# Kernel optimization log

Hardware: AMD Instinct MI355X
Metric: run time of the kernel (lower is better)

## Reference

```python
import jax, jax.numpy as jnp
import numpy as np

D = 256          # d_model
NH = 8           # n_heads
HD = D // NH
LEV = 3          # n_levels
NP = 4           # n_points
DFF = 1024       # d_ffn
B = 8            # batch
LQ = 3600        # 60*60 queries (hardcoded in get_reference_points)
SHAPES = np.array([[60, 60], [30, 30], [15, 15]], dtype=np.int64)
LIN = int((SHAPES[:, 0] * SHAPES[:, 1]).sum())  # 4725
START = np.concatenate([[0], np.cumsum(SHAPES[:, 0] * SHAPES[:, 1])[:-1]]).astype(np.int64)


def setup_inputs() -> dict:
    key = jax.random.key(0)
    ks = iter(jax.random.split(key, 32))
    def lin(k, o, i):
        return jax.random.normal(k, (o, i), jnp.float32) * 0.02
    return {
        "tgt": jax.random.normal(next(ks), (LQ, B, D), jnp.float32),
        "query_pos": jax.random.normal(next(ks), (1, 1, D), jnp.float32),
        "src": jax.random.normal(next(ks), (B, LIN, D), jnp.float32),
        "src_spatial_shapes": jnp.asarray(SHAPES),
        "level_start_index": jnp.asarray(START),
        "in_proj_w": lin(next(ks), 3 * D, D),
        "in_proj_b": jnp.zeros((3 * D,), jnp.float32),
        "out_proj_w": lin(next(ks), D, D),
        "out_proj_b": jnp.zeros((D,), jnp.float32),
        "samp_off_w": lin(next(ks), NH * LEV * NP * 2, D),
        "samp_off_b": jax.random.normal(next(ks), (NH * LEV * NP * 2,), jnp.float32) * 0.5,
        "attn_w_w": lin(next(ks), NH * LEV * NP, D),
        "attn_w_b": jnp.zeros((NH * LEV * NP,), jnp.float32),
        "value_proj_w": lin(next(ks), D, D),
        "value_proj_b": jnp.zeros((D,), jnp.float32),
        "cross_out_w": lin(next(ks), D, D),
        "cross_out_b": jnp.zeros((D,), jnp.float32),
        "ln1_g": jnp.ones((D,), jnp.float32), "ln1_b": jnp.zeros((D,), jnp.float32),
        "ln2_g": jnp.ones((D,), jnp.float32), "ln2_b": jnp.zeros((D,), jnp.float32),
        "ln3_g": jnp.ones((D,), jnp.float32), "ln3_b": jnp.zeros((D,), jnp.float32),
        "ffn_w1": lin(next(ks), DFF, D), "ffn_b1": jnp.zeros((DFF,), jnp.float32),
        "ffn_w2": lin(next(ks), D, DFF), "ffn_b2": jnp.zeros((D,), jnp.float32),
    }


def _ln(x, g, b, eps=1e-5):
    m = x.mean(-1, keepdims=True)
    v = ((x - m) ** 2).mean(-1, keepdims=True)
    return (x - m) * jax.lax.rsqrt(v + eps) * g + b


def _self_attn(q_in, k_in, v_in, wqkv, bqkv, wo, bo):
    # torch nn.MultiheadAttention semantics, inputs laid out (seq, batch, embed)
    S, N, _ = q_in.shape
    q = (q_in @ wqkv[:D].T + bqkv[:D]).reshape(S, N, NH, HD)
    k = (k_in @ wqkv[D:2 * D].T + bqkv[D:2 * D]).reshape(S, N, NH, HD)
    v = (v_in @ wqkv[2 * D:].T + bqkv[2 * D:]).reshape(S, N, NH, HD)
    logits = jnp.einsum('snhd,tnhd->nhst', q, k) / np.sqrt(HD).astype(np.float32)
    a = jax.nn.softmax(logits, -1)
    ctx = jnp.einsum('nhst,tnhd->snhd', a, v).reshape(S, N, D)
    return ctx @ wo.T + bo


def _bilinear(v_l, loc, Hl, Wl):
    # v_l: [B, NH, Hl*Wl, HD]; loc: [B, NH, LQ, NP, 2] normalized in [0,1]
    # grid_sample(align_corners=False, padding=zeros): pixel = loc*size - 0.5
    x = loc[..., 0] * Wl - 0.5
    y = loc[..., 1] * Hl - 0.5
    x0 = jnp.floor(x); y0 = jnp.floor(y)
    fx = x - x0; fy = y - y0
    x0 = x0.astype(jnp.int32); y0 = y0.astype(jnp.int32)
    def corner(yi, xi, w):
        valid = ((xi >= 0) & (xi < Wl) & (yi >= 0) & (yi < Hl)).astype(v_l.dtype)
        idx = jnp.clip(yi, 0, Hl - 1) * Wl + jnp.clip(xi, 0, Wl - 1)
        b, h, lq, p = idx.shape
        g = jnp.take_along_axis(v_l, idx.reshape(b, h, lq * p)[..., None], axis=2)
        return g.reshape(b, h, lq, p, HD) * (w * valid)[..., None]
    return (corner(y0, x0, (1 - fx) * (1 - fy))
            + corner(y0, x0 + 1, fx * (1 - fy))
            + corner(y0 + 1, x0, (1 - fx) * fy)
            + corner(y0 + 1, x0 + 1, fx * fy))


def _msdeform(query, ref, src, wso, bso, waw, baw, wv, bv, wo, bo):
    Bq, Lq, _ = query.shape
    value = (src @ wv.T + bv).reshape(Bq, LIN, NH, HD).transpose(0, 2, 1, 3)  # [B,NH,LIN,HD]
    off = (query @ wso.T + bso).reshape(Bq, Lq, NH, LEV, NP, 2)
    aw = (query @ waw.T + baw).reshape(Bq, Lq, NH, LEV * NP)
    aw = jax.nn.softmax(aw, -1).reshape(Bq, Lq, NH, LEV, NP)
    normalizer = jnp.asarray(SHAPES[:, ::-1].copy(), jnp.float32)  # (W, H) per level
    loc = ref[:, :, None, :, None, :] + off / normalizer[None, None, None, :, None, :]
    out = jnp.zeros((Bq, NH, Lq, HD), query.dtype)
    for l in range(LEV):
        Hl, Wl = int(SHAPES[l, 0]), int(SHAPES[l, 1])
        s = int(START[l])
        v_l = value[:, :, s:s + Hl * Wl]
        loc_l = loc[:, :, :, l].transpose(0, 2, 1, 3, 4)      # [B,NH,LQ,NP,2]
        sampled = _bilinear(v_l, loc_l, Hl, Wl)               # [B,NH,LQ,NP,HD]
        out = out + (sampled * aw[:, :, :, l].transpose(0, 2, 1, 3)[..., None]).sum(3)
    out = out.transpose(0, 2, 1, 3).reshape(Bq, Lq, D)
    return out @ wo.T + bo


def _reference_points():
    Hh = Ww = 60
    ys = (jnp.arange(Hh, dtype=jnp.float32) + 0.5) / Hh
    xs = (jnp.arange(Ww, dtype=jnp.float32) + 0.5) / Ww
    yy, xx = jnp.meshgrid(ys, xs, indexing='ij')
    ref = jnp.stack([xx.reshape(-1), yy.reshape(-1)], -1)[None]  # [1, 3600, 2]
    return jnp.broadcast_to(ref[:, :, None, :], (1, Hh * Ww, LEV, 2))


def reference(tgt, query_pos, src, src_spatial_shapes, level_start_index,
              in_proj_w, in_proj_b, out_proj_w, out_proj_b,
              samp_off_w, samp_off_b, attn_w_w, attn_w_b,
              value_proj_w, value_proj_b, cross_out_w, cross_out_b,
              ln1_g, ln1_b, ln2_g, ln2_b, ln3_g, ln3_b,
              ffn_w1, ffn_b1, ffn_w2, ffn_b2):
    # dropout layers are identity (eval mode). spatial shapes are static metadata
    # (SHAPES/START) since slicing sizes must be static under jit.
    q = (tgt + query_pos).transpose(1, 0, 2)
    tgt2 = _self_attn(q, q, tgt.transpose(1, 0, 2), in_proj_w, in_proj_b, out_proj_w, out_proj_b)
    t = _ln(tgt + tgt2.transpose(1, 0, 2), ln2_g, ln2_b)
    ref = _reference_points()
    tq = t.transpose(1, 0, 2)  # permute(1,0,2) -> [B, LQ, D]
    tgt2 = _msdeform(tq + query_pos, ref, src, samp_off_w, samp_off_b,
                     attn_w_w, attn_w_b, value_proj_w, value_proj_b,
                     cross_out_w, cross_out_b)
    tq = _ln(tq + tgt2, ln1_g, ln1_b)
    ff = jax.nn.relu(tq @ ffn_w1.T + ffn_b1) @ ffn_w2.T + ffn_b2
    tq = _ln(tq + ff, ln3_g, ln3_b)
    return tq.transpose(1, 0, 2)  # [LQ, B, D]
```

## Files before the change

### kernel.cpp

```cpp
#include <hip/hip_runtime.h>
#include <hip/hip_bf16.h>
#include <cstddef>
#include <cstdint>

#define D_MODEL 256
#define NHEAD   8
#define HDIM    32
#define NLEV    3
#define NPNT    4
#define DFF     1024
#define BATCH   8
#define LQ      3600
#define LIN     4725
#define MROWS   (BATCH*LQ)

typedef short bf16x8 __attribute__((ext_vector_type(8)));
typedef float f32x4  __attribute__((ext_vector_type(4)));

__device__ __forceinline__ unsigned short f2b(float x) {
    unsigned int u = __float_as_uint(x);
    unsigned int r = (u + 0x7fffu + ((u >> 16) & 1u)) >> 16;
    return (unsigned short)r;
}
__device__ __forceinline__ float b2f(unsigned short s) {
    return __uint_as_float(((unsigned int)s) << 16);
}

#define GLDS16(g, l) __builtin_amdgcn_global_load_lds( \
    (const __attribute__((address_space(1))) void*)(g), \
    (__attribute__((address_space(3))) void*)(l), 16, 0, 0)

#define WAIT_VM0()  asm volatile("s_waitcnt vmcnt(0)" ::: "memory")
#define WAIT_LGKM0() asm volatile("s_waitcnt lgkmcnt(0)" ::: "memory")

#define WTOT 991232
__global__ __launch_bounds__(256) void prep_kernel(
    const float* __restrict__ tgt, unsigned short* __restrict__ tgtb,
    const float* __restrict__ srcf, unsigned short* __restrict__ srcb,
    const float* __restrict__ w_in, const float* __restrict__ w_out,
    const float* __restrict__ w_val, const float* __restrict__ w_cross,
    const float* __restrict__ w_so, const float* __restrict__ w_aw,
    const float* __restrict__ w_f1, const float* __restrict__ w_f2,
    unsigned short* __restrict__ wdst,
    const float* __restrict__ qp, const float* __restrict__ so_b,
    const float* __restrict__ aw_b, float* __restrict__ qpv)
{
    const int bid = blockIdx.x;
    const int tid = threadIdx.x;
    if (bid < 7200) {
        int i = bid * 256 + tid;
        float4 v = ((const float4*)tgt)[i];
        ushort4 o; o.x = f2b(v.x); o.y = f2b(v.y); o.z = f2b(v.z); o.w = f2b(v.w);
        ((ushort4*)tgtb)[i] = o;
    } else if (bid < 16650) {
        int i = (bid - 7200) * 256 + tid;
        float4 v = ((const float4*)srcf)[i];
        ushort4 o; o.x = f2b(v.x); o.y = f2b(v.y); o.z = f2b(v.z); o.w = f2b(v.w);
        ((ushort4*)srcb)[i] = o;
    } else if (bid < 17618) {
        int idx = ((bid - 16650) * 256 + tid) * 4;
        if (idx >= WTOT) return;
        const float* src; int off;
        if      (idx < 196608) { src = w_in;    off = idx; }
        else if (idx < 262144) { src = w_out;   off = idx - 196608; }
        else if (idx < 327680) { src = w_val;   off = idx - 262144; }
        else if (idx < 393216) { src = w_cross; off = idx - 327680; }
        else if (idx < 442368) { src = w_so;    off = idx - 393216; }
        else if (idx < 466944) { src = w_aw;    off = idx - 442368; }
        else if (idx < 729088) { src = w_f1;    off = idx - 466944; }
        else                   { src = w_f2;    off = idx - 729088; }
        float4 v = *(const float4*)(src + off);
        ushort4 o; o.x = f2b(v.x); o.y = f2b(v.y); o.z = f2b(v.z); o.w = f2b(v.w);
        *(ushort4*)(wdst + idx) = o;
    } else {
        int o = (bid - 17618) * 256 + tid;
        if (o >= 768 + 192 + 96) return;
        const float* wrow;
        if (o < 768)       wrow = w_in + (size_t)o * D_MODEL;
        else if (o < 960)  wrow = w_so + (size_t)(o - 768) * D_MODEL;
        else               wrow = w_aw + (size_t)(o - 960) * D_MODEL;
        float acc = 0.f;
        for (int d = 0; d < D_MODEL; ++d) acc += qp[d] * wrow[d];
        qpv[o] = acc;
        if (o >= 768) {
            float bias = (o < 960) ? so_b[o - 768] : aw_b[o - 960];
            qpv[1056 + (o - 768)] = acc + bias;
        }
    }
}

__global__ __launch_bounds__(256) void gemm_bf16(
    const unsigned short* __restrict__ A,
    const unsigned short* __restrict__ W,
    const float* __restrict__ bias,
    const float* __restrict__ bias2, int b2lim,
    float* __restrict__ Cf, unsigned short* __restrict__ Cb,
    int M, int N, int K, int relu)
{
    __shared__ __align__(16) unsigned short As[2 * 128 * 32];
    __shared__ __align__(16) unsigned short Bs[2 * 128 * 32];
    const int tid  = threadIdx.x;
    const int wave = tid >> 6;
    const int lane = tid & 63;
    const int m0 = blockIdx.x * 128;
    const int n0 = blockIdx.y * 128;

    const int lr  = lane >> 2;
    const int lc8 = (lane & 3) * 8;
    int ar0 = m0 + wave * 32 + lr;      if (ar0 > M - 1) ar0 = M - 1;
    int ar1 = m0 + wave * 32 + 16 + lr; if (ar1 > M - 1) ar1 = M - 1;
    int br0 = n0 + wave * 32 + lr;      if (br0 > N - 1) br0 = N - 1;
    int br1 = n0 + wave * 32 + 16 + lr; if (br1 > N - 1) br1 = N - 1;
    const unsigned short* pa0 = A + (size_t)ar0 * K + lc8;
    const unsigned short* pa1 = A + (size_t)ar1 * K + lc8;
    const unsigned short* pb0 = W + (size_t)br0 * K + lc8;
    const unsigned short* pb1 = W + (size_t)br1 * K + lc8;
    unsigned short* la0 = As + wave * 1024;
    unsigned short* la1 = As + wave * 1024 + 512;
    unsigned short* lb0 = Bs + wave * 1024;
    unsigned short* lb1 = Bs + wave * 1024 + 512;

    const int wm = (wave >> 1) * 64;
    const int wn = (wave & 1) * 64;
    const int fr = lane & 15;
    const int fk = (lane >> 4) * 8;

    f32x4 acc[4][4] = {};

    for (int k0 = 0; k0 < K; k0 += 64) {
        GLDS16(pa0, la0); GLDS16(pa0 + 32, la0 + 4096);
        GLDS16(pa1, la1); GLDS16(pa1 + 32, la1 + 4096);
        GLDS16(pb0, lb0); GLDS16(pb0 + 32, lb0 + 4096);
        GLDS16(pb1, lb1); GLDS16(pb1 + 32, lb1 + 4096);
        pa0 += 64; pa1 += 64; pb0 += 64; pb1 += 64;
        __syncthreads();
#pragma unroll
        for (int p = 0; p < 2; ++p) {
            bf16x8 af[4], bfv[4];
#pragma unroll
            for (int i = 0; i < 4; ++i)
                af[i] = *(const bf16x8*)&As[p * 4096 + (wm + i * 16 + fr) * 32 + fk];
#pragma unroll
            for (int j = 0; j < 4; ++j)
                bfv[j] = *(const bf16x8*)&Bs[p * 4096 + (wn + j * 16 + fr) * 32 + fk];
#pragma unroll
            for (int i = 0; i < 4; ++i)
#pragma unroll
                for (int j = 0; j < 4; ++j)
                    acc[i][j] = __builtin_amdgcn_mfma_f32_16x16x32_bf16(
                        af[i], bfv[j], acc[i][j], 0, 0, 0);
        }
        __syncthreads();
    }

    const int quad = lane >> 4;
#pragma unroll
    for (int j = 0; j < 4; ++j) {
        const int col = n0 + wn + j * 16 + fr;
        if (col >= N) continue;
        float bv = 0.f;
        if (bias) bv += bias[col];
        if (bias2 && col < b2lim) bv += bias2[col];
#pragma unroll
        for (int i = 0; i < 4; ++i) {
#pragma unroll
            for (int r = 0; r < 4; ++r) {
                const int row = m0 + wm + i * 16 + quad * 4 + r;
                if (row >= M) continue;
                float v = acc[i][j][r] + bv;
                if (relu) v = fmaxf(v, 0.f);
                if (Cf) Cf[(size_t)row * N + col] = v;
                if (Cb) Cb[(size_t)row * N + col] = f2b(v);
            }
        }
    }
}

__global__ __launch_bounds__(256) void ln2_offs_kernel(
    const unsigned short* __restrict__ A,
    const unsigned short* __restrict__ Wo,
    const float* __restrict__ bo,
    const float* __restrict__ resid,
    const float* __restrict__ g2, const float* __restrict__ b2g,
    float* __restrict__ tout,
    const unsigned short* __restrict__ Wso,
    const float* __restrict__ cbias,
    float* __restrict__ comb)
{
    __shared__ __align__(16) unsigned short Wc[16384];
    __shared__ float2 red[128];
    const int tid  = threadIdx.x;
    const int wave = tid >> 6;
    const int lane = tid & 63;
    const int m0 = blockIdx.x * 32;
    const int fr   = lane & 15;
    const int quad = lane >> 4;
    const int xm   = fr & 7;

#pragma unroll
    for (int j = 0; j < 4; ++j) {
        const int c  = wave * 4 + j;
        const int rA = c * 2 + (lane >> 5);
        const int k8 = (lane & 31) ^ (rA & 7);
        GLDS16(A + (size_t)(m0 + rA) * 256 + k8 * 8, Wc + c * 512);
    }
    int w1off[8], w4off[8];
#pragma unroll
    for (int j = 0; j < 8; ++j) {
        const int c  = wave * 8 + j;
        const int n1 = c * 2 + (lane >> 5);
        const int k1 = (lane & 31) ^ (n1 & 7);
        w1off[j] = n1 * 256 + k1 * 8;
        const int n4 = (n1 < 32) ? n1 : 31;
        const int k4 = (lane & 31) ^ (n4 & 7);
        w4off[j] = n4 * 256 + k4 * 8;
    }
    __syncthreads();
    bf16x8 af[2][8];
#pragma unroll
    for (int i = 0; i < 2; ++i)
#pragma unroll
        for (int s = 0; s < 8; ++s)
            af[i][s] = *(const bf16x8*)&Wc[((i * 16 + fr) * 32 + ((s * 4 + quad) ^ xm)) * 8];
    WAIT_LGKM0();
    __syncthreads();

#pragma unroll
    for (int j = 0; j < 8; ++j)
        GLDS16(Wo + w1off[j], Wc + (wave * 8 + j) * 512);
    f32x4 accc[4][2] = {};
    for (int c = 0; c < 4; ++c) {
        WAIT_VM0();
        bf16x8 bv[8];
#pragma unroll
        for (int s = 0; s < 8; ++s)
            bv[s] = *(const bf16x8*)&Wc[((wave * 16 + fr) * 32 + ((s * 4 + quad) ^ xm)) * 8];
        WAIT_LGKM0();
        if (c < 3) {
#pragma unroll
            for (int j = 0; j < 8; ++j)
                GLDS16(Wo + (size_t)(c + 1) * 16384 + w1off[j], Wc + (wave * 8 + j) * 512);
        }
#pragma unroll
        for (int s = 0; s < 8; ++s) {
            accc[c][0] = __builtin_amdgcn_mfma_f32_16x16x32_bf16(af[0][s], bv[s], accc[c][0], 0, 0, 0);
            accc[c][1] = __builtin_amdgcn_mfma_f32_16x16x32_bf16(af[1][s], bv[s], accc[c][1], 0, 0, 0);
        }
    }

    float rs[2][4], rq[2][4];
#pragma unroll
    for (int x = 0; x < 2; ++x) {
#pragma unroll
        for (int r = 0; r < 4; ++r) {
            const int row = m0 + x * 16 + quad * 4 + r;
            float s = 0.f, q = 0.f;
#pragma unroll
            for (int c = 0; c < 4; ++c) {
                const int col = c * 64 + wave * 16 + fr;
                float v = accc[c][x][r] + bo[col] + resid[(size_t)row * 256 + col];
                accc[c][x][r] = v;
                s += v; q += v * v;
            }
            rs[x][r] = s; rq[x][r] = q;
        }
    }
#pragma unroll
    for (int off = 1; off < 16; off <<= 1) {
#pragma unroll
        for (int x = 0; x < 2; ++x)
#pragma unroll
            for (int r = 0; r < 4; ++r) {
                rs[x][r] += __shfl_xor(rs[x][r], off);
                rq[x][r] += __shfl_xor(rq[x][r], off);
            }
    }
    if ((lane & 15) == 0) {
#pragma unroll
        for (int x = 0; x < 2; ++x)
#pragma unroll
            for (int r = 0; r < 4; ++r)
                red[wave * 32 + x * 16 + quad * 4 + r] = make_float2(rs[x][r], rq[x][r]);
    }
    __syncthreads();
#pragma unroll
    for (int x = 0; x < 2; ++x) {
#pragma unroll
        for (int r = 0; r < 4; ++r) {
            const int rl = x * 16 + quad * 4 + r;
            const float2 t0 = red[rl], t1 = red[32 + rl], t2r = red[64 + rl], t3 = red[96 + rl];
            const float sum = t0.x + t1.x + t2r.x + t3.x;
            const float sq  = t0.y + t1.y + t2r.y + t3.y;
            const float mean = sum * (1.f / 256.f);
            const float var  = sq * (1.f / 256.f) - mean * mean;
            const float inv  = rsqrtf(var + 1e-5f);
            const int row = m0 + rl;
#pragma unroll
            for (int c = 0; c < 4; ++c) {
                const int col = c * 64 + wave * 16 + fr;
                const float val = (accc[c][x][r] - mean) * inv * g2[col] + b2g[col];
                tout[(size_t)row * 256 + col] = val;
                const int g8 = col >> 3;
                Wc[rl * 256 + ((g8 ^ (rl & 7)) << 3) + (col & 7)] = f2b(val);
            }
        }
    }
    __syncthreads();
#pragma unroll
    for (int i = 0; i < 2; ++i)
#pragma unroll
        for (int s = 0; s < 8; ++s)
            af[i][s] = *(const bf16x8*)&Wc[((i * 16 + fr) * 32 + ((s * 4 + quad) ^ xm)) * 8];
    WAIT_LGKM0();
    __syncthreads();

#pragma unroll
    for (int j = 0; j < 8; ++j)
        GLDS16(Wso + w1off[j], Wc + (wave * 8 + j) * 512);
    f32x4 accP[5][2] = {};
    for (int c = 0; c < 5; ++c) {
        WAIT_VM0();
        bf16x8 bv[8];
#pragma unroll
        for (int s = 0; s < 8; ++s)
            bv[s] = *(const bf16x8*)&Wc[((wave * 16 + fr) * 32 + ((s * 4 + quad) ^ xm)) * 8];
        WAIT_LGKM0();
        if (c < 4) {
            if (c < 3) {
#pragma unroll
                for (int j = 0; j < 8; ++j)
                    GLDS16(Wso + (size_t)(c + 1) * 16384 + w1off[j], Wc + (wave * 8 + j) * 512);
            } else {
#pragma unroll
                for (int j = 0; j < 8; ++j)
                    GLDS16(Wso + (size_t)4 * 16384 + w4off[j], Wc + (wave * 8 + j) * 512);
            }
        }
#pragma unroll
        for (int s = 0; s < 8; ++s) {
            accP[c][0] = __builtin_amdgcn_mfma_f32_16x16x32_bf16(af[0][s], bv[s], accP[c][0], 0, 0, 0);
            accP[c][1] = __builtin_amdgcn_mfma_f32_16x16x32_bf16(af[1][s], bv[s], accP[c][1], 0, 0, 0);
        }
    }

#pragma unroll
    for (int c = 0; c < 5; ++c) {
        const int col = c * 64 + wave * 16 + fr;
        if (col >= 288) continue;
        const float cb = cbias[col];
#pragma unroll
        for (int x = 0; x < 2; ++x)
#pragma unroll
            for (int r = 0; r < 4; ++r) {
                const int row = m0 + x * 16 + quad * 4 + r;
                comb[(size_t)row * 288 + col] = accP[c][x][r] + cb;
            }
    }
}

__global__ __launch_bounds__(256) void cross_ffn_kernel(
    const unsigned short* __restrict__ A,
    const unsigned short* __restrict__ Wcr,
    const float* __restrict__ bcr,
    const float* __restrict__ resid1,
    const float* __restrict__ g1, const float* __restrict__ b1g,
    float* __restrict__ t2,
    const unsigned short* __restrict__ W1,
    const float* __restrict__ b1,
    const unsigned short* __restrict__ W2,
    const float* __restrict__ b2,
    const float* __restrict__ g3, const float* __restrict__ b3g,
    float* __restrict__ outf)
{
    __shared__ __align__(16) unsigned short Wc[16384];
    __shared__ __align__(16) unsigned short hid[2304];
    const int tid  = threadIdx.x;
    const int wave = tid >> 6;
    const int lane = tid & 63;
    const int m0 = blockIdx.x * 32;
    const int fr   = lane & 15;
    const int quad = lane >> 4;
    const int xm   = fr & 7;
    float2* red = (float2*)hid;

#pragma unroll
    for (int j = 0; j < 4; ++j) {
        const int c  = wave * 4 + j;
        const int rA = c * 2 + (lane >> 5);
        const int k8 = (lane & 31) ^ (rA & 7);
        GLDS16(A + (size_t)(m0 + rA) * 256 + k8 * 8, Wc + c * 512);
    }
    int w1off[8], w2off[8];
#pragma unroll
    for (int j = 0; j < 8; ++j) {
        const int c  = wave * 8 + j;
        const int n1 = c * 2 + (lane >> 5);
        const int k1 = (lane & 31) ^ (n1 & 7);
        w1off[j] = n1 * 256 + k1 * 8;
        const int n2 = c * 8 + (lane >> 3);
        const int k2 = (lane & 7) ^ (n2 & 7);
        w2off[j] = n2 * 1024 + k2 * 8;
    }
    __syncthreads();
    bf16x8 af[2][8];
#pragma unroll
    for (int i = 0; i < 2; ++i)
#pragma unroll
        for (int s = 0; s < 8; ++s)
            af[i][s] = *(const bf16x8*)&Wc[((i * 16 + fr) * 32 + ((s * 4 + quad) ^ xm)) * 8];
    WAIT_LGKM0();
    __syncthreads();

#pragma unroll
    for (int j = 0; j < 8; ++j)
        GLDS16(Wcr + w1off[j], Wc + (wave * 8 + j) * 512);
    f32x4 accc[4][2] = {};
    for (int c = 0; c < 4; ++c) {
        WAIT_VM0();
        bf16x8 bv[8];
#pragma unroll
        for (int s = 0; s < 8; ++s)
            bv[s] = *(const bf16x8*)&Wc[((wave * 16 + fr) * 32 + ((s * 4 + quad) ^ xm)) * 8];
        WAIT_LGKM0();
        if (c < 3) {
#pragma unroll
            for (int j = 0; j < 8; ++j)
                GLDS16(Wcr + (size_t)(c + 1) * 16384 + w1off[j], Wc + (wave * 8 + j) * 512);
        }
#pragma unroll
        for (int s = 0; s < 8; ++s) {
            accc[c][0] = __builtin_amdgcn_mfma_f32_16x16x32_bf16(af[0][s], bv[s], accc[c][0], 0, 0, 0);
            accc[c][1] = __builtin_amdgcn_mfma_f32_16x16x32_bf16(af[1][s], bv[s], accc[c][1], 0, 0, 0);
        }
    }

    float rs[2][4], rq[2][4];
#pragma unroll
    for (int x = 0; x < 2; ++x) {
#pragma unroll
        for (int r = 0; r < 4; ++r) {
            const int row = m0 + x * 16 + quad * 4 + r;
            float s = 0.f, q = 0.f;
#pragma unroll
            for (int c = 0; c < 4; ++c) {
                const int col = c * 64 + wave * 16 + fr;
                float v = accc[c][x][r] + bcr[col] + resid1[(size_t)row * 256 + col];
                accc[c][x][r] = v;
                s += v; q += v * v;
            }
            rs[x][r] = s; rq[x][r] = q;
        }
    }
#pragma unroll
    for (int off = 1; off < 16; off <<= 1) {
#pragma unroll
        for (int x = 0; x < 2; ++x)
#pragma unroll
            for (int r = 0; r < 4; ++r) {
                rs[x][r] += __shfl_xor(rs[x][r], off);
                rq[x][r] += __shfl_xor(rq[x][r], off);
            }
    }
    if ((lane & 15) == 0) {
#pragma unroll
        for (int x = 0; x < 2; ++x)
#pragma unroll
            for (int r = 0; r < 4; ++r)
                red[wave * 32 + x * 16 + quad * 4 + r] = make_float2(rs[x][r], rq[x][r]);
    }
    __syncthreads();
#pragma unroll
    for (int x = 0; x < 2; ++x) {
#pragma unroll
        for (int r = 0; r < 4; ++r) {
            const int rl = x * 16 + quad * 4 + r;
            const float2 t0 = red[rl], t1 = red[32 + rl], t2r = red[64 + rl], t3 = red[96 + rl];
            const float sum = t0.x + t1.x + t2r.x + t3.x;
            const float sq  = t0.y + t1.y + t2r.y + t3.y;
            const float mean = sum * (1.f / 256.f);
            const float var  = sq * (1.f / 256.f) - mean * mean;
            const float inv  = rsqrtf(var + 1e-5f);
            const int row = m0 + rl;
#pragma unroll
            for (int c = 0; c < 4; ++c) {
                const int col = c * 64 + wave * 16 + fr;
                const float val = (accc[c][x][r] - mean) * inv * g1[col] + b1g[col];
                t2[(size_t)row * 256 + col] = val;
                const int g8 = col >> 3;
                Wc[rl * 256 + ((g8 ^ (rl & 7)) << 3) + (col & 7)] = f2b(val);
            }
        }
    }
    __syncthreads();
#pragma unroll
    for (int i = 0; i < 2; ++i)
#pragma unroll
        for (int s = 0; s < 8; ++s)
            af[i][s] = *(const bf16x8*)&Wc[((i * 16 + fr) * 32 + ((s * 4 + quad) ^ xm)) * 8];
    WAIT_LGKM0();
    __syncthreads();

#pragma unroll
    for (int j = 0; j < 8; ++j)
        GLDS16(W1 + w1off[j], Wc + (wave * 8 + j) * 512);
    WAIT_VM0();

    f32x4 acc2[2][4] = {};

    for (int h = 0; h < 16; ++h) {
        bf16x8 bv[8];
#pragma unroll
        for (int s = 0; s < 8; ++s)
            bv[s] = *(const bf16x8*)&Wc[((wave * 16 + fr) * 32 + ((s * 4 + quad) ^ xm)) * 8];
        WAIT_LGKM0();
#pragma unroll
        for (int j = 0; j < 8; ++j)
            GLDS16(W2 + (size_t)h * 64 + w2off[j], Wc + (wave * 8 + j) * 512);
        f32x4 acc1[2] = {};
#pragma unroll
        for (int s = 0; s < 8; ++s) {
            acc1[0] = __builtin_amdgcn_mfma_f32_16x16x32_bf16(af[0][s], bv[s], acc1[0], 0, 0, 0);
            acc1[1] = __builtin_amdgcn_mfma_f32_16x16x32_bf16(af[1][s], bv[s], acc1[1], 0, 0, 0);
        }
        const float bias1 = b1[h * 64 + wave * 16 + fr];
#pragma unroll
        for (int i = 0; i < 2; ++i)
#pragma unroll
            for (int r = 0; r < 4; ++r) {
                float v = fmaxf(acc1[i][r] + bias1, 0.f);
                hid[(i * 16 + quad * 4 + r) * 72 + wave * 16 + fr] = f2b(v);
            }
        __syncthreads();
#pragma unroll
        for (int s = 0; s < 2; ++s) {
            bf16x8 a2[2], b2v[4];
#pragma unroll
            for (int j2 = 0; j2 < 4; ++j2) {
                const int nb = wave * 64 + j2 * 16 + fr;
                b2v[j2] = *(const bf16x8*)&Wc[(nb * 8 + ((s * 4 + quad) ^ xm)) * 8];
            }
#pragma unroll
            for (int i = 0; i < 2; ++i)
                a2[i] = *(const bf16x8*)&hid[(i * 16 + fr) * 72 + s * 32 + quad * 8];
            if (s == 1) {
                WAIT_LGKM0();
                if (h < 15) {
#pragma unroll
                    for (int j = 0; j < 8; ++j)
                        GLDS16(W1 + (size_t)(h + 1) * 16384 + w1off[j], Wc + (wave * 8 + j) * 512);
                }
            }
#pragma unroll
            for (int i = 0; i < 2; ++i)
#pragma unroll
                for (int j2 = 0; j2 < 4; ++j2)
                    acc2[i][j2] = __builtin_amdgcn_mfma_f32_16x16x32_bf16(
                        a2[i], b2v[j2], acc2[i][j2], 0, 0, 0);
        }
        __syncthreads();
    }

    const int colbase = wave * 64;
#pragma unroll
    for (int x = 0; x < 2; ++x) {
#pragma unroll
        for (int r = 0; r < 4; ++r) {
            const int row = m0 + x * 16 + quad * 4 + r;
            float s = 0.f, q = 0.f;
#pragma unroll
            for (int y = 0; y < 4; ++y) {
                const int col = colbase + y * 16 + fr;
                float v = acc2[x][y][r] + b2[col] + t2[(size_t)row * 256 + col];
                acc2[x][y][r] = v;
                s += v; q += v * v;
            }
            rs[x][r] = s; rq[x][r] = q;
        }
    }
#pragma unroll
    for (int off = 1; off < 16; off <<= 1) {
#pragma unroll
        for (int x = 0; x < 2; ++x)
#pragma unroll
            for (int r = 0; r < 4; ++r) {
                rs[x][r] += __shfl_xor(rs[x][r], off);
                rq[x][r] += __shfl_xor(rq[x][r], off);
            }
    }
    if ((lane & 15) == 0) {
#pragma unroll
        for (int x = 0; x < 2; ++x)
#pragma unroll
            for (int r = 0; r < 4; ++r)
                red[wave * 32 + x * 16 + quad * 4 + r] = make_float2(rs[x][r], rq[x][r]);
    }
    __syncthreads();
#pragma unroll
    for (int x = 0; x < 2; ++x) {
#pragma unroll
        for (int r = 0; r < 4; ++r) {
            const int rl = x * 16 + quad * 4 + r;
            const float2 t0 = red[rl], t1 = red[32 + rl], t2r = red[64 + rl], t3 = red[96 + rl];
            const float sum = t0.x + t1.x + t2r.x + t3.x;
            const float sq  = t0.y + t1.y + t2r.y + t3.y;
            const float mean = sum * (1.f / 256.f);
            const float var  = sq * (1.f / 256.f) - mean * mean;
            const float inv  = rsqrtf(var + 1e-5f);
            const int row = m0 + rl;
#pragma unroll
            for (int y = 0; y < 4; ++y) {
                const int col = colbase + y * 16 + fr;
                outf[(size_t)row * 256 + col] = (acc2[x][y][r] - mean) * inv * g3[col] + b3g[col];
            }
        }
    }
}

__global__ __launch_bounds__(256) void self_attn_kernel(
    const unsigned short* __restrict__ qkv, unsigned short* __restrict__ ctx)
{
    __shared__ float sh[8][768];
    __shared__ float ls[8][8][8];
    __shared__ __align__(16) unsigned short ob[2048];
    const int n = blockIdx.x;
    const int t = threadIdx.x;

    const unsigned short* base = qkv + (size_t)n * 8 * 768;
#pragma unroll
    for (int i = 0; i < 3; ++i) {
        const int idx = (i * 256 + t) * 8;
        bf16x8 v = *(const bf16x8*)&base[idx];
        const int s = idx / 768;
        const int c = idx - s * 768;
#pragma unroll
        for (int j = 0; j < 8; ++j)
            sh[s][c + j] = b2f((unsigned short)v[j]);
    }
    __syncthreads();
    const int h = t >> 5, j = t & 31;
#pragma unroll
    for (int pair = j; pair < 64; pair += 32) {
        const int s = pair >> 3, tt = pair & 7;
        float acc = 0.f;
#pragma unroll
        for (int d = 0; d < 32; ++d)
            acc += sh[s][h * 32 + d] * sh[tt][256 + h * 32 + d];
        ls[h][s][tt] = acc * 0.17677669529663687f;
    }
    __syncthreads();
    if (t < 64) {
        const int hh = t >> 3, s = t & 7;
        float mx = -1e30f;
        for (int tt = 0; tt < 8; ++tt) mx = fmaxf(mx, ls[hh][s][tt]);
        float sum = 0.f;
        for (int tt = 0; tt < 8; ++tt) { float e = expf(ls[hh][s][tt] - mx); ls[hh][s][tt] = e; sum += e; }
        const float inv = 1.f / sum;
        for (int tt = 0; tt < 8; ++tt) ls[hh][s][tt] *= inv;
    }
    __syncthreads();
#pragma unroll
    for (int s = 0; s < 8; ++s) {
        float acc = 0.f;
#pragma unroll
        for (int tt = 0; tt < 8; ++tt)
            acc += ls[h][s][tt] * sh[tt][512 + h * 32 + j];
        ob[s * 256 + t] = f2b(acc);
    }
    __syncthreads();
    ((bf16x8*)ctx)[(size_t)n * 256 + t] = ((const bf16x8*)ob)[t];
}

__global__ __launch_bounds__(256) void msdeform_kernel(
    const unsigned short* __restrict__ value,
    const float* __restrict__ comb,
    unsigned short* __restrict__ out)
{
    const int bid = blockIdx.x;
    const int b   = bid & 7;
    const int lq0 = (bid >> 3) * 4;
    const int r    = threadIdx.x >> 6;
    const int lane = threadIdx.x & 63;
    const int h = lane >> 3;
    const int l = lane & 7;
    const int lq = lq0 + r;
    const int m = lq * 8 + b;

    const float* offp = comb + (size_t)m * 288 + h * 24;
    const float* awp  = comb + (size_t)m * 288 + 192 + h * 12;
    float off[24], aw[12];
#pragma unroll
    for (int i = 0; i < 6; ++i) *(float4*)&off[i * 4] = ((const float4*)offp)[i];
#pragma unroll
    for (int i = 0; i < 3; ++i) *(float4*)&aw[i * 4] = ((const float4*)awp)[i];

    float mx = aw[0];
#pragma unroll
    for (int i = 1; i < 12; ++i) mx = fmaxf(mx, aw[i]);
    float se = 0.f;
#pragma unroll
    for (int i = 0; i < 12; ++i) { aw[i] = __expf(aw[i] - mx); se += aw[i]; }
    const float inv = 1.f / se;

    const float refx = ((lq % 60) + 0.5f) * (1.f / 60.f);
    const float refy = ((lq / 60) + 0.5f) * (1.f / 60.f);
    const int HW[3] = {60, 30, 15};
    const int ST[3] = {0, 3600, 4500};

    const unsigned short* vbase = value + (size_t)b * LIN * 256 + h * 32 + l * 4;

    float a0 = 0.f, a1 = 0.f, a2 = 0.f, a3 = 0.f;
#pragma unroll
    for (int lev = 0; lev < NLEV; ++lev) {
        const int Wl = HW[lev], s0 = ST[lev];
        const float fWl = (float)Wl;
#pragma unroll
        for (int p = 0; p < NPNT; ++p) {
            const int pt = lev * 4 + p;
            const float ox = off[lev * 8 + p * 2];
            const float oy = off[lev * 8 + p * 2 + 1];
            const float px = refx * fWl + ox - 0.5f;
            const float py = refy * fWl + oy - 0.5f;
            const float x0f = floorf(px), y0f = floorf(py);
            const float fx = px - x0f, fy = py - y0f;
            const int x0 = (int)x0f, y0 = (int)y0f;
            const float aww = aw[pt] * inv;
            const float vx0 = (x0 >= 0 && x0 < Wl) ? 1.f : 0.f;
            const float vx1 = (x0 >= -1 && x0 < Wl - 1) ? 1.f : 0.f;
            const float vy0 = (y0 >= 0 && y0 < Wl) ? 1.f : 0.f;
            const float vy1 = (y0 >= -1 && y0 < Wl - 1) ? 1.f : 0.f;
            const int xc0 = min(max(x0, 0), Wl - 1);
            const int xc1 = min(max(x0 + 1, 0), Wl - 1);
            const int yc0 = min(max(y0, 0), Wl - 1);
            const int yc1 = min(max(y0 + 1, 0), Wl - 1);
            const int sx  = xc1 - xc0;
            const int syW = (yc1 - yc0) * Wl;
            const int i00 = s0 + yc0 * Wl + xc0;
            const float w00 = (1.f - fx) * (1.f - fy) * aww * vx0 * vy0;
            const float w01 = fx * (1.f - fy) * aww * vx1 * vy0;
            const float w10 = (1.f - fx) * fy * aww * vx0 * vy1;
            const float w11 = fx * fy * aww * vx1 * vy1;
            const int i01 = i00 + sx;
            const int i10 = i00 + syW;
            const int i11 = i10 + sx;
            const ushort4 g00 = *(const ushort4*)(vbase + (size_t)i00 * 256);
            const ushort4 g01 = *(const ushort4*)(vbase + (size_t)i01 * 256);
            const ushort4 g10 = *(const ushort4*)(vbase + (size_t)i10 * 256);
            const ushort4 g11 = *(const ushort4*)(vbase + (size_t)i11 * 256);
            a0 += b2f(g00.x) * w00 + b2f(g01.x) * w01 + b2f(g10.x) * w10 + b2f(g11.x) * w11;
            a1 += b2f(g00.y) * w00 + b2f(g01.y) * w01 + b2f(g10.y) * w10 + b2f(g11.y) * w11;
            a2 += b2f(g00.z) * w00 + b2f(g01.z) * w01 + b2f(g10.z) * w10 + b2f(g11.z) * w11;
            a3 += b2f(g00.w) * w00 + b2f(g01.w) * w01 + b2f(g10.w) * w10 + b2f(g11.w) * w11;
        }
    }
    ushort4 o;
    o.x = f2b(a0); o.y = f2b(a1); o.z = f2b(a2); o.w = f2b(a3);
    *(ushort4*)(out + (size_t)m * 256 + h * 32 + l * 4) = o;
}

extern "C" void kernel_launch(void* const* d_in, const int* in_sizes, int n_in,
                              void* d_out, int out_size, void* d_ws, size_t ws_size,
                              hipStream_t stream)
{
    (void)in_sizes; (void)n_in; (void)out_size; (void)ws_size;
    const float* tgt          = (const float*)d_in[0];
    const float* qp           = (const float*)d_in[1];
    const float* src          = (const float*)d_in[2];
    const float* in_proj_w    = (const float*)d_in[5];
    const float* in_proj_b    = (const float*)d_in[6];
    const float* out_proj_w   = (const float*)d_in[7];
    const float* out_proj_b   = (const float*)d_in[8];
    const float* samp_off_w   = (const float*)d_in[9];
    const float* samp_off_b   = (const float*)d_in[10];
    const float* attn_w_w     = (const float*)d_in[11];
    const float* attn_w_b     = (const float*)d_in[12];
    const float* value_proj_w = (const float*)d_in[13];
    const float* value_proj_b = (const float*)d_in[14];
    const float* cross_out_w  = (const float*)d_in[15];
    const float* cross_out_b  = (const float*)d_in[16];
    const float* ln1_g = (const float*)d_in[17];
    const float* ln1_b = (const float*)d_in[18];
    const float* ln2_g = (const float*)d_in[19];
    const float* ln2_b = (const float*)d_in[20];
    const float* ln3_g = (const float*)d_in[21];
    const float* ln3_b = (const float*)d_in[22];
    const float* ffn_w1 = (const float*)d_in[23];
    const float* ffn_b1 = (const float*)d_in[24];
    const float* ffn_w2 = (const float*)d_in[25];
    const float* ffn_b2 = (const float*)d_in[26];
    float* out = (float*)d_out;

    float* ws    = (float*)d_ws;
    float* t     = ws;
    float* t2    = ws + 7372800;
    float* comb  = ws + 14745600;
    float* qpv   = ws + 23040000;
    float* cbias = qpv + 1056;

    unsigned short* bws    = (unsigned short*)((char*)d_ws + 92165376);
    unsigned short* s1     = bws;
    unsigned short* tgtb   = s1;
    unsigned short* ctxb   = s1;
    unsigned short* s2     = bws + 7372800;
    unsigned short* qkvb   = s2;
    unsigned short* valueb = s2;
    unsigned short* msoutb = s2 + 9676800;
    unsigned short* srcb   = bws + 36864000;
    unsigned short* wtsb   = bws + 46540800;

    prep_kernel<<<17623, 256, 0, stream>>>(tgt, tgtb, src, srcb,
                                           in_proj_w, out_proj_w, value_proj_w,
                                           cross_out_w, samp_off_w, attn_w_w,
                                           ffn_w1, ffn_w2, wtsb,
                                           qp, samp_off_b, attn_w_b, qpv);
    gemm_bf16<<<dim3(225, 6), 256, 0, stream>>>(tgtb, wtsb + 0, in_proj_b, qpv, 512,
                                                nullptr, qkvb, MROWS, 768, 256, 0);
    self_attn_kernel<<<3600, 256, 0, stream>>>(qkvb, ctxb);
    ln2_offs_kernel<<<900, 256, 0, stream>>>(ctxb, wtsb + 196608, out_proj_b,
                                             tgt, ln2_g, ln2_b, t,
                                             wtsb + 393216, cbias, comb);
    gemm_bf16<<<dim3(296, 2), 256, 0, stream>>>(srcb, wtsb + 262144, value_proj_b, nullptr, 0,
                                                nullptr, valueb, BATCH * LIN, 256, 256, 0);
    msdeform_kernel<<<7200, 256, 0, stream>>>(valueb, comb, msoutb);
    cross_ffn_kernel<<<900, 256, 0, stream>>>(msoutb, wtsb + 327680, cross_out_b,
                                              t, ln1_g, ln1_b, t2,
                                              wtsb + 466944, ffn_b1,
                                              wtsb + 729088, ffn_b2,
                                              ln3_g, ln3_b, out);
}
```

Measured before the change: 444.5 us.

## Fuse QKV projection and self-attention into the out-proj/LN2/offsets kernel

Moves the QKV GEMM and the 8-token per-query self-attention into the existing out-projection/LayerNorm/sampling-offset kernel, so each 32-row tile computes Q, K, V into shared memory and writes the attention context straight into the A-operand buffer. This drops two kernel launches and the global round trips for the QKV and context tensors. In exchange the fused kernel uses more shared memory (two extra 32x264 bf16 tiles), which may lower occupancy, and it runs the serial QKV chunks inside the block.

```diff
diff --git a/kernel.cpp b/kernel.cpp
--- a/kernel.cpp
+++ b/kernel.cpp
@@ -176,8 +176,11 @@
     }
 }
 
-__global__ __launch_bounds__(256) void ln2_offs_kernel(
+__global__ __launch_bounds__(256) void qkv_attn_ln2_offs_kernel(
     const unsigned short* __restrict__ A,
+    const unsigned short* __restrict__ Win,
+    const float* __restrict__ bin,
+    const float* __restrict__ qpv,
     const unsigned short* __restrict__ Wo,
     const float* __restrict__ bo,
     const float* __restrict__ resid,
@@ -188,6 +191,8 @@
     float* __restrict__ comb)
 {
     __shared__ __align__(16) unsigned short Wc[16384];
+    __shared__ __align__(16) unsigned short qt[32 * 264];
+    __shared__ __align__(16) unsigned short kvt[32 * 264];
     __shared__ float2 red[128];
     const int tid  = threadIdx.x;
     const int wave = tid >> 6;
@@ -227,6 +232,118 @@
 
 #pragma unroll
     for (int j = 0; j < 8; ++j)
+        GLDS16(Win + w1off[j], Wc + (wave * 8 + j) * 512);
+
+#define QCHUNK(CG, PF) {                                                     \
+        WAIT_VM0();                                                          \
+        bf16x8 bv[8];                                                        \
+        _Pragma("unroll")                                                    \
+        for (int s = 0; s < 8; ++s)                                          \
+            bv[s] = *(const bf16x8*)&Wc[((wave * 16 + fr) * 32 + ((s * 4 + quad) ^ xm)) * 8]; \
+        WAIT_LGKM0();                                                        \
+        if (PF) {                                                            \
+            _Pragma("unroll")                                                \
+            for (int j = 0; j < 8; ++j)                                      \
+                GLDS16(Win + (size_t)((CG) + 1) * 16384 + w1off[j], Wc + (wave * 8 + j) * 512); \
+        }                                                                    \
+        _Pragma("unroll")                                                    \
+        for (int s = 0; s < 8; ++s) {                                        \
+            acc[(CG) & 3][0] = __builtin_amdgcn_mfma_f32_16x16x32_bf16(af[0][s], bv[s], acc[(CG) & 3][0], 0, 0, 0); \
+            acc[(CG) & 3][1] = __builtin_amdgcn_mfma_f32_16x16x32_bf16(af[1][s], bv[s], acc[(CG) & 3][1], 0, 0, 0); \
+        }                                                                    \
+    }
+
+#define QKV_EPI(P, TILE) {                                                   \
+        _Pragma("unroll")                                                    \
+        for (int x = 0; x < 2; ++x)                                          \
+        _Pragma("unroll")                                                    \
+        for (int r = 0; r < 4; ++r) {                                        \
+            const int rl = x * 16 + quad * 4 + r;                            \
+            _Pragma("unroll")                                                \
+            for (int c = 0; c < 4; ++c) {                                    \
+                const int col  = c * 64 + wave * 16 + fr;                    \
+                const int gcol = (P) * 256 + col;                            \
+                float v = acc[c][x][r] + bin[gcol];                          \
+                if ((P) < 2) v += qpv[gcol];                                 \
+                (TILE)[rl * 264 + col] = f2b(v);                             \
+            }                                                                \
+        }                                                                    \
+    }
+
+    {
+        f32x4 acc[4][2] = {};
+#pragma unroll
+        for (int c = 0; c < 4; ++c) QCHUNK(c, 1)
+        QKV_EPI(0, qt)
+    }
+    {
+        f32x4 acc[4][2] = {};
+#pragma unroll
+        for (int c = 4; c < 8; ++c) QCHUNK(c, 1)
+        QKV_EPI(1, kvt)
+    }
+    __syncthreads();
+
+    const int g  = wave;
+    const int ah = lane >> 3;
+    const int si = lane & 7;
+    float p[8];
+    {
+        float qreg[32];
+#pragma unroll
+        for (int d = 0; d < 32; ++d)
+            qreg[d] = b2f(qt[(g * 8 + si) * 264 + ah * 32 + d]);
+        float mx = -1e30f;
+#pragma unroll
+        for (int ti = 0; ti < 8; ++ti) {
+            float a = 0.f;
+#pragma unroll
+            for (int d = 0; d < 32; ++d)
+                a += qreg[d] * b2f(kvt[(g * 8 + ti) * 264 + ah * 32 + d]);
+            a *= 0.17677669529663687f;
+            p[ti] = a;
+            mx = fmaxf(mx, a);
+        }
+        float sum = 0.f;
+#pragma unroll
+        for (int ti = 0; ti < 8; ++ti) { p[ti] = expf(p[ti] - mx); sum += p[ti]; }
+        const float inv = 1.f / sum;
+#pragma unroll
+        for (int ti = 0; ti < 8; ++ti) p[ti] *= inv;
+    }
+    __syncthreads();
+
+    {
+        f32x4 acc[4][2] = {};
+#pragma unroll
+        for (int c = 8; c < 12; ++c) QCHUNK(c, (c < 11))
+        QKV_EPI(2, kvt)
+    }
+    __syncthreads();
+
+    {
+        const int rl = g * 8 + si;
+#pragma unroll
+        for (int d = 0; d < 32; ++d) {
+            float a = 0.f;
+#pragma unroll
+            for (int ti = 0; ti < 8; ++ti)
+                a += p[ti] * b2f(kvt[(g * 8 + ti) * 264 + ah * 32 + d]);
+            const int col = ah * 32 + d;
+            Wc[rl * 256 + (((col >> 3) ^ (rl & 7)) << 3) + (col & 7)] = f2b(a);
+        }
+    }
+    __syncthreads();
+#pragma unroll
+    for (int i = 0; i < 2; ++i)
+#pragma unroll
+        for (int s = 0; s < 8; ++s)
+            af[i][s] = *(const bf16x8*)&Wc[((i * 16 + fr) * 32 + ((s * 4 + quad) ^ xm)) * 8];
+    WAIT_LGKM0();
+    __syncthreads();
+
+#pragma unroll
+    for (int j = 0; j < 8; ++j)
         GLDS16(Wo + w1off[j], Wc + (wave * 8 + j) * 512);
     f32x4 accc[4][2] = {};
     for (int c = 0; c < 4; ++c) {
@@ -247,7 +364,6 @@
             accc[c][1] = __builtin_amdgcn_mfma_f32_16x16x32_bf16(af[1][s], bv[s], accc[c][1], 0, 0, 0);
         }
     }
-
     float rs[2][4], rq[2][4];
 #pragma unroll
     for (int x = 0; x < 2; ++x) {
@@ -342,7 +458,6 @@
             accP[c][1] = __builtin_amdgcn_mfma_f32_16x16x32_bf16(af[1][s], bv[s], accP[c][1], 0, 0, 0);
         }
     }
-
 #pragma unroll
     for (int c = 0; c < 5; ++c) {
         const int col = c * 64 + wave * 16 + fr;
@@ -356,6 +471,8 @@
                 comb[(size_t)row * 288 + col] = accP[c][x][r] + cb;
             }
     }
+#undef QCHUNK
+#undef QKV_EPI
 }
 
 __global__ __launch_bounds__(256) void cross_ffn_kernel(
@@ -614,60 +731,6 @@
             }
         }
     }
-}
-
-__global__ __launch_bounds__(256) void self_attn_kernel(
-    const unsigned short* __restrict__ qkv, unsigned short* __restrict__ ctx)
-{
-    __shared__ float sh[8][768];
-    __shared__ float ls[8][8][8];
-    __shared__ __align__(16) unsigned short ob[2048];
-    const int n = blockIdx.x;
-    const int t = threadIdx.x;
-
-    const unsigned short* base = qkv + (size_t)n * 8 * 768;
-#pragma unroll
-    for (int i = 0; i < 3; ++i) {
-        const int idx = (i * 256 + t) * 8;
-        bf16x8 v = *(const bf16x8*)&base[idx];
-        const int s = idx / 768;
-        const int c = idx - s * 768;
-#pragma unroll
-        for (int j = 0; j < 8; ++j)
-            sh[s][c + j] = b2f((unsigned short)v[j]);
-    }
-    __syncthreads();
-    const int h = t >> 5, j = t & 31;
-#pragma unroll
-    for (int pair = j; pair < 64; pair += 32) {
-        const int s = pair >> 3, tt = pair & 7;
-        float acc = 0.f;
-#pragma unroll
-        for (int d = 0; d < 32; ++d)
-            acc += sh[s][h * 32 + d] * sh[tt][256 + h * 32 + d];
-        ls[h][s][tt] = acc * 0.17677669529663687f;
-    }
-    __syncthreads();
-    if (t < 64) {
-        const int hh = t >> 3, s = t & 7;
-        float mx = -1e30f;
-        for (int tt = 0; tt < 8; ++tt) mx = fmaxf(mx, ls[hh][s][tt]);
-        float sum = 0.f;
-        for (int tt = 0; tt < 8; ++tt) { float e = expf(ls[hh][s][tt] - mx); ls[hh][s][tt] = e; sum += e; }
-        const float inv = 1.f / sum;
-        for (int tt = 0; tt < 8; ++tt) ls[hh][s][tt] *= inv;
-    }
-    __syncthreads();
-#pragma unroll
-    for (int s = 0; s < 8; ++s) {
-        float acc = 0.f;
-#pragma unroll
-        for (int tt = 0; tt < 8; ++tt)
-            acc += ls[h][s][tt] * sh[tt][512 + h * 32 + j];
-        ob[s * 256 + t] = f2b(acc);
-    }
-    __syncthreads();
-    ((bf16x8*)ctx)[(size_t)n * 256 + t] = ((const bf16x8*)ob)[t];
 }
 
 __global__ __launch_bounds__(256) void msdeform_kernel(
@@ -797,11 +860,8 @@
     float* cbias = qpv + 1056;
 
     unsigned short* bws    = (unsigned short*)((char*)d_ws + 92165376);
-    unsigned short* s1     = bws;
-    unsigned short* tgtb   = s1;
-    unsigned short* ctxb   = s1;
+    unsigned short* tgtb   = bws;
     unsigned short* s2     = bws + 7372800;
-    unsigned short* qkvb   = s2;
     unsigned short* valueb = s2;
     unsigned short* msoutb = s2 + 9676800;
     unsigned short* srcb   = bws + 36864000;
@@ -812,14 +872,12 @@
                                            cross_out_w, samp_off_w, attn_w_w,
                                            ffn_w1, ffn_w2, wtsb,
                                            qp, samp_off_b, attn_w_b, qpv);
-    gemm_bf16<<<dim3(225, 6), 256, 0, stream>>>(tgtb, wtsb + 0, in_proj_b, qpv, 512,
-                                                nullptr, qkvb, MROWS, 768, 256, 0);
-    self_attn_kernel<<<3600, 256, 0, stream>>>(qkvb, ctxb);
-    ln2_offs_kernel<<<900, 256, 0, stream>>>(ctxb, wtsb + 196608, out_proj_b,
-                                             tgt, ln2_g, ln2_b, t,
-                                             wtsb + 393216, cbias, comb);
     gemm_bf16<<<dim3(296, 2), 256, 0, stream>>>(srcb, wtsb + 262144, value_proj_b, nullptr, 0,
                                                 nullptr, valueb, BATCH * LIN, 256, 256, 0);
+    qkv_attn_ln2_offs_kernel<<<900, 256, 0, stream>>>(
+        tgtb, wtsb + 0, in_proj_b, qpv,
+        wtsb + 196608, out_proj_b, tgt, ln2_g, ln2_b, t,
+        wtsb + 393216, cbias, comb);
     msdeform_kernel<<<7200, 256, 0, stream>>>(valueb, comb, msoutb);
     cross_ffn_kernel<<<900, 256, 0, stream>>>(msoutb, wtsb + 327680, cross_out_b,
                                               t, ln1_g, ln1_b, t2,
```

After: 427.4 us. 3.8% less time.
